# Performance work log

Hardware: AMD Instinct MI355X
Metric: run time of the kernel (lower is better)

## Reference

```python
import jax, jax.numpy as jnp
import numpy as np

N_V, N_R = 50000, 500
E_VV, E_VI, E_IV = 400000, 100000, 100000
D_V, D_R = 6, 1
HID, HEADS, OUT = 32, 2, 64
L2 = HID * HEADS  # input dim of layer 2 = hidden_dim * heads = 64


def _gatv2(x_src, x_dst, src, dst, Wl, bl, Wr, br, att, bias, heads, outc, add_self_loops):
    """PyG GATv2Conv: e_ij = att . leaky_relu(Wl x_j + Wr x_i), softmax over dst segments,
    out_i = sum_j alpha_ij * (Wl x_j). add_self_loops also removes pre-existing self loops
    (emulated with a validity mask to keep static shapes)."""
    n_src, n_dst = x_src.shape[0], x_dst.shape[0]
    hl = (x_src @ Wl + bl).reshape(n_src, heads, outc)  # source projection (messages)
    hr = (x_dst @ Wr + br).reshape(n_dst, heads, outc)  # target projection
    if add_self_loops:
        n_loop = min(n_src, n_dst)  # PyG uses min over bipartite sizes
        loop = jnp.arange(n_loop)
        valid = jnp.concatenate([src != dst, jnp.ones((n_loop,), bool)])
        src = jnp.concatenate([src, loop])
        dst = jnp.concatenate([dst, loop])
    else:
        valid = jnp.ones(src.shape, bool)
    m_src = hl[src]                                        # [E, H, C]
    m_dst = hr[dst]                                        # [E, H, C]
    e = (jax.nn.leaky_relu(m_src + m_dst, 0.2) * att).sum(-1)  # [E, H]
    e_masked = jnp.where(valid[:, None], e, -jnp.inf)
    emax = jax.ops.segment_max(e_masked, dst, num_segments=n_dst)
    emax = jnp.where(jnp.isfinite(emax), emax, 0.0)
    w = jnp.where(valid[:, None], jnp.exp(e - emax[dst]), 0.0)
    denom = jax.ops.segment_sum(w, dst, num_segments=n_dst)
    alpha = w / (denom[dst] + 1e-16)                       # [E, H]
    out = jax.ops.segment_sum(alpha[..., None] * m_src, dst, num_segments=n_dst)
    return out.reshape(n_dst, heads * outc) + bias         # concat (heads=1: identity)


def _ln(x, w, b):
    mu = jnp.mean(x, -1, keepdims=True)
    var = jnp.mean((x - mu) ** 2, -1, keepdims=True)
    return (x - mu) * jax.lax.rsqrt(var + 1e-5) * w + b


def setup_inputs() -> dict:
    key = jax.random.key(0)
    ks = jax.random.split(key, 50)
    rn = lambda i, shape, s=0.1: jax.random.normal(ks[i], shape, jnp.float32) * s
    inp = dict(
        x_veh=jax.random.normal(ks[0], (N_V, D_V), jnp.float32),
        x_rsu=jax.random.normal(ks[1], (N_R, D_R), jnp.float32),
        ei_v2v=jax.random.randint(ks[2], (2, E_VV), 0, N_V),
        ei_v2i=jnp.stack([jax.random.randint(ks[3], (E_VI,), 0, N_V),
                          jax.random.randint(ks[4], (E_VI,), 0, N_R)]),
        ei_i2v=jnp.stack([jax.random.randint(ks[5], (E_IV,), 0, N_R),
                          jax.random.randint(ks[6], (E_IV,), 0, N_V)]),
        # conv1 (heads=2, concat=True)
        p1v_Wl=rn(7, (D_V, L2)), p1v_bl=rn(8, (L2,)), p1v_Wr=rn(9, (D_V, L2)), p1v_br=rn(10, (L2,)), p1v_att=rn(11, (HEADS, HID)), p1v_b=rn(12, (L2,)),
        p1i_Wl=rn(13, (D_V, L2)), p1i_bl=rn(14, (L2,)), p1i_Wr=rn(15, (D_R, L2)), p1i_br=rn(16, (L2,)), p1i_att=rn(17, (HEADS, HID)), p1i_b=rn(18, (L2,)),
        p1r_Wl=rn(19, (D_R, L2)), p1r_bl=rn(20, (L2,)), p1r_Wr=rn(21, (D_V, L2)), p1r_br=rn(22, (L2,)), p1r_att=rn(23, (HEADS, HID)), p1r_b=rn(24, (L2,)),
        # conv2 (heads=1, concat=False)
        p2v_Wl=rn(25, (L2, OUT)), p2v_bl=rn(26, (OUT,)), p2v_Wr=rn(27, (L2, OUT)), p2v_br=rn(28, (OUT,)), p2v_att=rn(29, (1, OUT)), p2v_b=rn(30, (OUT,)),
        p2i_Wl=rn(31, (L2, OUT)), p2i_bl=rn(32, (OUT,)), p2i_Wr=rn(33, (L2, OUT)), p2i_br=rn(34, (OUT,)), p2i_att=rn(35, (1, OUT)), p2i_b=rn(36, (OUT,)),
        p2r_Wl=rn(37, (L2, OUT)), p2r_bl=rn(38, (OUT,)), p2r_Wr=rn(39, (L2, OUT)), p2r_br=rn(40, (OUT,)), p2r_att=rn(41, (1, OUT)), p2r_b=rn(42, (OUT,)),
        lnv_w=jnp.ones((OUT,), jnp.float32), lnv_b=jnp.zeros((OUT,), jnp.float32),
        lnr_w=jnp.ones((OUT,), jnp.float32), lnr_b=jnp.zeros((OUT,), jnp.float32),
    )
    return inp


def reference(x_veh, x_rsu, ei_v2v, ei_v2i, ei_i2v,
              p1v_Wl, p1v_bl, p1v_Wr, p1v_br, p1v_att, p1v_b,
              p1i_Wl, p1i_bl, p1i_Wr, p1i_br, p1i_att, p1i_b,
              p1r_Wl, p1r_bl, p1r_Wr, p1r_br, p1r_att, p1r_b,
              p2v_Wl, p2v_bl, p2v_Wr, p2v_br, p2v_att, p2v_b,
              p2i_Wl, p2i_bl, p2i_Wr, p2i_br, p2i_att, p2i_b,
              p2r_Wl, p2r_bl, p2r_Wr, p2r_br, p2r_att, p2r_b,
              lnv_w, lnv_b, lnr_w, lnr_b):
    # ---- HeteroConv layer 1 (aggr='sum') ----
    v_v2v = _gatv2(x_veh, x_veh, ei_v2v[0], ei_v2v[1], p1v_Wl, p1v_bl, p1v_Wr, p1v_br, p1v_att, p1v_b, HEADS, HID, True)
    r_v2i = _gatv2(x_veh, x_rsu, ei_v2i[0], ei_v2i[1], p1i_Wl, p1i_bl, p1i_Wr, p1i_br, p1i_att, p1i_b, HEADS, HID, False)
    v_i2v = _gatv2(x_rsu, x_veh, ei_i2v[0], ei_i2v[1], p1r_Wl, p1r_bl, p1r_Wr, p1r_br, p1r_att, p1r_b, HEADS, HID, False)
    h_veh = jax.nn.elu(v_v2v + v_i2v)
    h_rsu = jax.nn.elu(r_v2i)
    # dropout(p=0.2) is identity in eval mode
    # ---- HeteroConv layer 2 (heads=1, add_self_loops default True) ----
    v2 = (_gatv2(h_veh, h_veh, ei_v2v[0], ei_v2v[1], p2v_Wl, p2v_bl, p2v_Wr, p2v_br, p2v_att, p2v_b, 1, OUT, True)
          + _gatv2(h_rsu, h_veh, ei_i2v[0], ei_i2v[1], p2r_Wl, p2r_bl, p2r_Wr, p2r_br, p2r_att, p2r_b, 1, OUT, True))
    r2 = _gatv2(h_veh, h_rsu, ei_v2i[0], ei_v2i[1], p2i_Wl, p2i_bl, p2i_Wr, p2i_br, p2i_att, p2i_b, 1, OUT, True)
    return _ln(v2, lnv_w, lnv_b), _ln(r2, lnr_w, lnr_b)
```

## Files before the change

kernel.cpp:

```cpp
#include <hip/hip_runtime.h>
#include <hip/hip_fp16.h>
#include <math.h>
#include <float.h>

#define NV 50000
#define NR 500
#define EVV 400000
#define EVI 100000
#define EIV 100000

#define CB_VV 0
#define CB_VI 50000
#define CB_IV 50500
#define CNT_LEN 100500
#define RB_VV 0
#define RB_VI 50004
#define RB_IV 50508
#define RP_LEN 100512
#define TILE 1024
#define T_VV 49
#define T_IV 49
#define T_TOT 99
#define HB4 586
#define FB4 586
#define PB 12500
#define GBV 2048
#define NBQ 1563
#define RSB 16

__global__ void hist_all_kernel(const int* __restrict__ vv_s, const int* __restrict__ vv_d,
                                const int* __restrict__ vi_d, const int* __restrict__ iv_d,
                                unsigned* __restrict__ cnt_all, unsigned* __restrict__ rank_all) {
  int t0 = blockIdx.x * 1024 + threadIdx.x;
  #pragma unroll
  for (int j = 0; j < 4; ++j) {
    int e = t0 + j * 256;
    if (e < EVV) {
      int s = vv_s[e], d = vv_d[e];
      if (s != d) rank_all[e] = atomicAdd(&cnt_all[CB_VV + d], 1u);
    } else if (e < EVV + EVI) {
      rank_all[e] = atomicAdd(&cnt_all[CB_VI + vi_d[e - EVV]], 1u);
    } else if (e < EVV + EVI + EIV) {
      rank_all[e] = atomicAdd(&cnt_all[CB_IV + iv_d[e - EVV - EVI]], 1u);
    }
  }
}

__device__ __forceinline__ void tile_decode(int b, int& cb, int& rb, int& n, int& base,
                                            int& topo, int& lt) {
  topo = (b < T_VV) ? 0 : (b == T_VV) ? 1 : 2;
  lt   = (topo == 0) ? b : (topo == 1) ? 0 : b - T_VV - 1;
  cb   = (topo == 0) ? CB_VV : (topo == 1) ? CB_VI : CB_IV;
  rb   = (topo == 0) ? RB_VV : (topo == 1) ? RB_VI : RB_IV;
  n    = (topo == 1) ? NR : NV;
  base = lt * TILE;
}

__global__ void tilesum_kernel(const unsigned* __restrict__ cnt_all, unsigned* __restrict__ tsum) {
  int cb, rb, n, base, topo, lt;
  tile_decode(blockIdx.x, cb, rb, n, base, topo, lt);
  int t = threadIdx.x, lane = t & 63, wid = t >> 6;
  unsigned s = 0;
  #pragma unroll
  for (int j = 0; j < 4; ++j) {
    int i = base + t + j * 256;
    if (i < n) s += cnt_all[cb + i];
  }
  #pragma unroll
  for (int off = 32; off > 0; off >>= 1) s += (unsigned)__shfl_xor((int)s, off, 64);
  __shared__ unsigned wt[4];
  if (lane == 0) wt[wid] = s;
  __syncthreads();
  if (t == 0) tsum[blockIdx.x] = wt[0] + wt[1] + wt[2] + wt[3];
}

__global__ void scanwrite_kernel(const unsigned* __restrict__ cnt_all,
                                 const unsigned* __restrict__ tsum,
                                 unsigned* __restrict__ rp_all) {
  int cb, rb, n, base, topo, lt;
  tile_decode(blockIdx.x, cb, rb, n, base, topo, lt);
  int t = threadIdx.x, lane = t & 63, wid = t >> 6;
  __shared__ unsigned sprefix;
  __shared__ unsigned wt[4];
  if (wid == 0) {
    int first = (topo == 0) ? 0 : (topo == 1) ? T_VV : T_VV + 1;
    int cntT  = (topo == 1) ? 1 : T_VV;
    unsigned tv = (lane < cntT) ? tsum[first + lane] : 0u;
    unsigned vp = (lane < lt) ? tv : 0u;
    unsigned vt = tv;
    #pragma unroll
    for (int off = 32; off > 0; off >>= 1) {
      vp += (unsigned)__shfl_xor((int)vp, off, 64);
      vt += (unsigned)__shfl_xor((int)vt, off, 64);
    }
    if (lane == 0) {
      sprefix = vp;
      if (lt == 0) rp_all[rb + n] = vt;
    }
  }
  int i0 = base + t * 4;
  unsigned c0 = 0, c1 = 0, c2 = 0, c3 = 0;
  if (i0 + 3 < n) {
    uint4 v = *(const uint4*)&cnt_all[cb + i0];
    c0 = v.x; c1 = v.y; c2 = v.z; c3 = v.w;
  } else if (i0 < n) {
    c0 = cnt_all[cb + i0];
    if (i0 + 1 < n) c1 = cnt_all[cb + i0 + 1];
    if (i0 + 2 < n) c2 = cnt_all[cb + i0 + 2];
  }
  unsigned s4 = c0 + c1 + c2 + c3;
  unsigned inc = s4;
  #pragma unroll
  for (int off = 1; off < 64; off <<= 1) {
    unsigned v = (unsigned)__shfl_up((int)inc, off, 64);
    if (lane >= off) inc += v;
  }
  if (lane == 63) wt[wid] = inc;
  __syncthreads();
  unsigned wb = sprefix;
  #pragma unroll
  for (int w = 0; w < 4; ++w) if (w < wid) wb += wt[w];
  unsigned p0 = wb + inc - s4;
  unsigned p1 = p0 + c0, p2 = p1 + c1, p3 = p2 + c2;
  if (i0 + 3 < n) {
    *(uint4*)&rp_all[rb + i0] = make_uint4(p0, p1, p2, p3);
  } else if (i0 < n) {
    rp_all[rb + i0] = p0;
    if (i0 + 1 < n) rp_all[rb + i0 + 1] = p1;
    if (i0 + 2 < n) rp_all[rb + i0 + 2] = p2;
  }
}

__global__ void fill_proj_kernel(const int* __restrict__ vv_s, const int* __restrict__ vv_d,
                                 const int* __restrict__ vi_s, const int* __restrict__ vi_d,
                                 const int* __restrict__ iv_s, const int* __restrict__ iv_d,
                                 const unsigned* __restrict__ rp_all,
                                 const unsigned* __restrict__ rank_all,
                                 int* __restrict__ src_all,
                                 const float* __restrict__ x,
                                 const float* __restrict__ W0, const float* __restrict__ b0,
                                 const float* __restrict__ W1, const float* __restrict__ b1,
                                 const float* __restrict__ W2, const float* __restrict__ b2,
                                 const float* __restrict__ W3, const float* __restrict__ b3,
                                 __half* __restrict__ out0, __half* __restrict__ out1,
                                 float* __restrict__ out2, float* __restrict__ out3) {
  if (blockIdx.x < FB4) {
    int t0 = blockIdx.x * 1024 + threadIdx.x;
    #pragma unroll
    for (int j = 0; j < 4; ++j) {
      int e = t0 + j * 256;
      if (e < EVV) {
        int s = vv_s[e], d = vv_d[e];
        if (s != d) {
          unsigned pos = rp_all[RB_VV + d] + rank_all[e];
          __builtin_nontemporal_store(s, &src_all[pos]);
        }
      } else if (e < EVV + EVI) {
        int i = e - EVV;
        unsigned pos = rp_all[RB_VI + vi_d[i]] + rank_all[e];
        __builtin_nontemporal_store(vi_s[i], &src_all[EVV + pos]);
      } else if (e < EVV + EVI + EIV) {
        int i = e - EVV - EVI;
        unsigned pos = rp_all[RB_IV + iv_d[i]] + rank_all[e];
        __builtin_nontemporal_store(iv_s[i], &src_all[EVV + EVI + pos]);
      }
    }
  } else {
    int t = (blockIdx.x - FB4) * 256 + threadIdx.x;
    if (t >= NV * 64) return;
    int row = t >> 6, c = t & 63;
    const float* xr = x + (size_t)row * 6;
    float x0 = xr[0], x1 = xr[1], x2 = xr[2], x3 = xr[3], x4 = xr[4], x5 = xr[5];
    float a0 = b0[c], a1 = b1[c], a2 = b2[c], a3 = b3[c];
    a0 = fmaf(x0, W0[0 * 64 + c], a0); a1 = fmaf(x0, W1[0 * 64 + c], a1);
    a2 = fmaf(x0, W2[0 * 64 + c], a2); a3 = fmaf(x0, W3[0 * 64 + c], a3);
    a0 = fmaf(x1, W0[1 * 64 + c], a0); a1 = fmaf(x1, W1[1 * 64 + c], a1);
    a2 = fmaf(x1, W2[1 * 64 + c], a2); a3 = fmaf(x1, W3[1 * 64 + c], a3);
    a0 = fmaf(x2, W0[2 * 64 + c], a0); a1 = fmaf(x2, W1[2 * 64 + c], a1);
    a2 = fmaf(x2, W2[2 * 64 + c], a2); a3 = fmaf(x2, W3[2 * 64 + c], a3);
    a0 = fmaf(x3, W0[3 * 64 + c], a0); a1 = fmaf(x3, W1[3 * 64 + c], a1);
    a2 = fmaf(x3, W2[3 * 64 + c], a2); a3 = fmaf(x3, W3[3 * 64 + c], a3);
    a0 = fmaf(x4, W0[4 * 64 + c], a0); a1 = fmaf(x4, W1[4 * 64 + c], a1);
    a2 = fmaf(x4, W2[4 * 64 + c], a2); a3 = fmaf(x4, W3[4 * 64 + c], a3);
    a0 = fmaf(x5, W0[5 * 64 + c], a0); a1 = fmaf(x5, W1[5 * 64 + c], a1);
    a2 = fmaf(x5, W2[5 * 64 + c], a2); a3 = fmaf(x5, W3[5 * 64 + c], a3);
    out0[t] = __float2half(a0);
    out1[t] = __float2half(a1);
    out2[t] = a2;
    out3[t] = a3;
  }
}

template <int R0>
__device__ __forceinline__ float redsum(float ee) {
  #pragma unroll
  for (int off = R0; off > 0; off >>= 1) ee += __shfl_xor(ee, off, 64);
  return ee;
}

__device__ __forceinline__ float4 cvt_h(int2 r) {
  __half2 ab = *(__half2*)&r.x;
  __half2 cd = *(__half2*)&r.y;
  float2 f0 = __half22float2(ab);
  float2 f1 = __half22float2(cd);
  return make_float4(f0.x, f0.y, f1.x, f1.y);
}
__device__ __forceinline__ float4 ldrow_h(const __half* p) { return cvt_h(*(const int2*)p); }

__device__ __forceinline__ void merge_groups(float& s, float4& a) {
  s   += __shfl_xor(s, 16, 64);
  a.x += __shfl_xor(a.x, 16, 64);
  a.y += __shfl_xor(a.y, 16, 64);
  a.z += __shfl_xor(a.z, 16, 64);
  a.w += __shfl_xor(a.w, 16, 64);
  s   += __shfl_xor(s, 32, 64);
  a.x += __shfl_xor(a.x, 32, 64);
  a.y += __shfl_xor(a.y, 32, 64);
  a.z += __shfl_xor(a.z, 32, 64);
  a.w += __shfl_xor(a.w, 32, 64);
}

template <int R0>
__device__ __forceinline__ void edge_acc(float4 p4, bool ok, float4 h, float4 a,
                                         float& s, float4& acc) {
  float vx = p4.x + h.x; vx = fmaxf(vx, 0.2f * vx);
  float vy = p4.y + h.y; vy = fmaxf(vy, 0.2f * vy);
  float vz = p4.z + h.z; vz = fmaxf(vz, 0.2f * vz);
  float vw = p4.w + h.w; vw = fmaxf(vw, 0.2f * vw);
  float ee = redsum<R0>(fmaf(vx, a.x, fmaf(vy, a.y, fmaf(vz, a.z, vw * a.w))));
  float w = ok ? __expf(ee) : 0.f;
  s += w;
  acc.x = fmaf(w, p4.x, acc.x);
  acc.y = fmaf(w, p4.y, acc.y);
  acc.z = fmaf(w, p4.z, acc.z);
  acc.w = fmaf(w, p4.w, acc.w);
}

template <int CHUNK, int NSLOT, int R0, bool MASK>
__device__ __forceinline__ void gat4_table(unsigned beg, unsigned end, unsigned slot,
                                           const int* __restrict__ srcs,
                                           const __half* __restrict__ tab, int q, int d,
                                           float4 h, float4 a, float& s, float4& acc) {
  for (unsigned i = beg + slot; i < end; i += NSLOT * CHUNK) {
    float4 p[CHUNK]; bool ok[CHUNK];
    #pragma unroll
    for (int j = 0; j < CHUNK; ++j) {
      unsigned idx = i + (unsigned)(j * NSLOT);
      int sv = (idx < end) ? srcs[idx] : 0;
      ok[j] = (idx < end) && (!MASK || sv != d);
      p[j] = ldrow_h(tab + (size_t)sv * 64 + 4 * q);
    }
    #pragma unroll
    for (int j = 0; j < CHUNK; ++j) edge_acc<R0>(p[j], ok[j], h, a, s, acc);
  }
}

__global__ __launch_bounds__(256)
void l1_all_kernel(const unsigned* __restrict__ rp_all, const int* __restrict__ src_all,
                   const __half* __restrict__ TA, const __half* __restrict__ TB,
                   const float* __restrict__ HRVV, const float* __restrict__ HRIV,
                   const float* __restrict__ x_rsu,
                   const float* __restrict__ Wl_iv, const float* __restrict__ bl_iv,
                   const float* __restrict__ att_vv, const float* __restrict__ att_iv,
                   const float* __restrict__ Wr_vi, const float* __restrict__ br_vi,
                   const float* __restrict__ att_vi,
                   const float* __restrict__ b_vv, const float* __restrict__ b_iv,
                   const float* __restrict__ b_vi,
                   float* __restrict__ ACCV, float* __restrict__ ACCR) {
  __shared__ float sS[4][64];
  __shared__ float4 sA[4][64];
  int tid = threadIdx.x, lane = tid & 63, wid = tid >> 6;
  int q = lane & 15, g = lane >> 4;
  if (blockIdx.x < GBV) {
    float4 av = *(const float4*)&att_vv[4 * q];
    float4 ai = *(const float4*)&att_iv[4 * q];
    float4 wli = *(const float4*)&Wl_iv[4 * q];
    float4 bli = *(const float4*)&bl_iv[4 * q];
    float4 bvv = *(const float4*)&b_vv[4 * q];
    float4 biv = *(const float4*)&b_iv[4 * q];
    float4 bb = make_float4(bvv.x + biv.x, bvv.y + biv.y, bvv.z + biv.z, bvv.w + biv.w);
    const int* src_iv = src_all + EVV + EVI;
    int d = blockIdx.x * 4 + wid;
    unsigned vb = 0, ve = 0, ib = 0, ie = 0;
    int psv0 = 0, psv1 = 0, pisv = 0;
    if (d < NV) {
      vb = rp_all[RB_VV + d]; ve = rp_all[RB_VV + d + 1];
      ib = rp_all[RB_IV + d]; ie = rp_all[RB_IV + d + 1];
      unsigned i0 = vb + (unsigned)g, i1 = i0 + 4;
      psv0 = (i0 < ve) ? src_all[i0] : 0;
      psv1 = (i1 < ve) ? src_all[i1] : 0;
      unsigned ii0 = ib + (unsigned)g;
      pisv = (ii0 < ie) ? src_iv[ii0] : 0;
    }
    while (d < NV) {
      int dn = d + GBV * 4;
      unsigned cvb = vb, cve = ve, cib = ib, cie = ie;
      int2 r0raw = *(const int2*)(TA + (size_t)psv0 * 64 + 4 * q);
      int2 r1raw = *(const int2*)(TA + (size_t)psv1 * 64 + 4 * q);
      float ixv = x_rsu[pisv];
      bool iok0 = (cib + (unsigned)g) < cie;
      if (dn < NV) {
        vb = rp_all[RB_VV + dn]; ve = rp_all[RB_VV + dn + 1];
        ib = rp_all[RB_IV + dn]; ie = rp_all[RB_IV + dn + 1];
      }
      float4 hv = *(const float4*)&HRVV[(size_t)d * 64 + 4 * q];
      float4 hi = *(const float4*)&HRIV[(size_t)d * 64 + 4 * q];
      float sv_ = 0.f; float4 av_ = make_float4(0.f, 0.f, 0.f, 0.f);
      edge_acc<4>(cvt_h(r0raw), (cvb + (unsigned)g) < cve, hv, av, sv_, av_);
      edge_acc<4>(cvt_h(r1raw), (cvb + (unsigned)g + 4) < cve, hv, av, sv_, av_);
      gat4_table<2, 4, 4, false>(cvb + 8, cve, (unsigned)g, src_all, TA, q, d, hv, av, sv_, av_);
      if (g == 0) {
        float4 p4 = ldrow_h(TA + (size_t)d * 64 + 4 * q);
        edge_acc<4>(p4, true, hv, av, sv_, av_);
      }
      merge_groups(sv_, av_);
      float si_ = 0.f; float4 ai_ = make_float4(0.f, 0.f, 0.f, 0.f);
      {
        float4 p4;
        p4.x = fmaf(ixv, wli.x, bli.x);
        p4.y = fmaf(ixv, wli.y, bli.y);
        p4.z = fmaf(ixv, wli.z, bli.z);
        p4.w = fmaf(ixv, wli.w, bli.w);
        edge_acc<4>(p4, iok0, hi, ai, si_, ai_);
      }
      for (unsigned i = cib + 4 + (unsigned)g; i < cie; i += 4) {
        int sv2 = src_iv[i];
        float xv2 = x_rsu[sv2];
        float4 p4;
        p4.x = fmaf(xv2, wli.x, bli.x);
        p4.y = fmaf(xv2, wli.y, bli.y);
        p4.z = fmaf(xv2, wli.z, bli.z);
        p4.w = fmaf(xv2, wli.w, bli.w);
        edge_acc<4>(p4, true, hi, ai, si_, ai_);
      }
      merge_groups(si_, ai_);
      if (dn < NV) {
        unsigned i0 = vb + (unsigned)g, i1 = i0 + 4;
        psv0 = (i0 < ve) ? src_all[i0] : 0;
        psv1 = (i1 < ve) ? src_all[i1] : 0;
        unsigned ii0 = ib + (unsigned)g;
        pisv = (ii0 < ie) ? src_iv[ii0] : 0;
      }
      if (g == 0) {
        float rv = 1.f / (sv_ + 1e-16f), ri = 1.f / (si_ + 1e-16f);
        float v0 = av_.x * rv + ai_.x * ri + bb.x;
        float v1 = av_.y * rv + ai_.y * ri + bb.y;
        float v2 = av_.z * rv + ai_.z * ri + bb.z;
        float v3 = av_.w * rv + ai_.w * ri + bb.w;
        float4 o;
        o.x = (v0 > 0.f) ? v0 : expm1f(v0);
        o.y = (v1 > 0.f) ? v1 : expm1f(v1);
        o.z = (v2 > 0.f) ? v2 : expm1f(v2);
        o.w = (v3 > 0.f) ? v3 : expm1f(v3);
        *(float4*)&ACCV[(size_t)d * 64 + 4 * q] = o;
      }
      d = dn;
    }
  } else {
    int d = (int)blockIdx.x - GBV;
    float xv = x_rsu[d];
    float4 wrv = *(const float4*)&Wr_vi[4 * q];
    float4 brv = *(const float4*)&br_vi[4 * q];
    float4 h;
    h.x = fmaf(xv, wrv.x, brv.x);
    h.y = fmaf(xv, wrv.y, brv.y);
    h.z = fmaf(xv, wrv.z, brv.z);
    h.w = fmaf(xv, wrv.w, brv.w);
    float4 a = *(const float4*)&att_vi[4 * q];
    float s_ = 0.f; float4 a_ = make_float4(0.f, 0.f, 0.f, 0.f);
    gat4_table<4, 16, 4, false>(rp_all[RB_VI + d], rp_all[RB_VI + d + 1],
                                (unsigned)(wid * 4 + g), src_all + EVV, TB, q, d,
                                h, a, s_, a_);
    merge_groups(s_, a_);
    if (wid != 0) { sS[wid][lane] = s_; sA[wid][lane] = a_; }
    __syncthreads();
    if (wid == 0) {
      #pragma unroll
      for (int w2 = 1; w2 < 4; ++w2) {
        s_ += sS[w2][lane];
        float4 t = sA[w2][lane];
        a_.x += t.x; a_.y += t.y; a_.z += t.z; a_.w += t.w;
      }
      if (g == 0) {
        float4 bvi = *(const float4*)&b_vi[4 * q];
        float inv = 1.f / (s_ + 1e-16f);
        float v0 = a_.x * inv + bvi.x;
        float v1 = a_.y * inv + bvi.y;
        float v2 = a_.z * inv + bvi.z;
        float v3 = a_.w * inv + bvi.w;
        float4 o;
        o.x = (v0 > 0.f) ? v0 : expm1f(v0);
        o.y = (v1 > 0.f) ? v1 : expm1f(v1);
        o.z = (v2 > 0.f) ? v2 : expm1f(v2);
        o.w = (v3 > 0.f) ? v3 : expm1f(v3);
        *(float4*)&ACCR[(size_t)d * 64 + 4 * q] = o;
      }
    }
  }
}

__global__ __launch_bounds__(256, 2)
void quad_proj_kernel(const float* __restrict__ ACCVin, const float* __restrict__ ACCR,
                      const float* __restrict__ W0, const float* __restrict__ b0,
                      const float* __restrict__ W1, const float* __restrict__ b1,
                      const float* __restrict__ W2, const float* __restrict__ b2,
                      const float* __restrict__ W3, const float* __restrict__ b3,
                      const float* __restrict__ W4, const float* __restrict__ b4,
                      const float* __restrict__ W5, const float* __restrict__ b5,
                      __half* __restrict__ O0, float* __restrict__ O1,
                      float* __restrict__ O2, __half* __restrict__ O3,
                      __half* __restrict__ S0o, float* __restrict__ S1o) {
  __shared__ float w0s[4096], w1s[4096], w2s[4096], w3s[4096], xtile[2048];
  int t = threadIdx.x;
  bool vehb = blockIdx.x < NBQ;
  const float* X = vehb ? ACCVin : ACCR;
  int n = vehb ? NV : NR;
  int base = (vehb ? (int)blockIdx.x : (int)blockIdx.x - NBQ) * 32;
  if (vehb) {
    for (int i = t; i < 4096; i += 256) { w0s[i] = W0[i]; w1s[i] = W1[i]; w2s[i] = W2[i]; w3s[i] = W3[i]; }
  } else {
    for (int i = t; i < 4096; i += 256) { w0s[i] = W4[i]; w1s[i] = W5[i]; }
  }
  for (int i = t; i < 2048; i += 256) {
    int row = base + (i >> 6);
    int rc = (row < n) ? row : (n - 1);
    xtile[i] = X[(size_t)rc * 64 + (i & 63)];
  }
  __syncthreads();
  int lane = t & 63, wid = t >> 6;
  int wr = wid * 8;
  int p = 4 * (lane & 15) + (lane >> 4);
  if (vehb) {
    float a0[8], a1[8], a2[8], a3[8];
    #pragma unroll
    for (int r = 0; r < 8; ++r) { a0[r] = 0.f; a1[r] = 0.f; a2[r] = 0.f; a3[r] = 0.f; }
    for (int kq = 0; kq < 16; ++kq) {
      int k = kq * 4;
      float u00 = w0s[(k + 0) * 64 + lane], u01 = w0s[(k + 1) * 64 + lane];
      float u02 = w0s[(k + 2) * 64 + lane], u03 = w0s[(k + 3) * 64 + lane];
      float u10 = w1s[(k + 0) * 64 + lane], u11 = w1s[(k + 1) * 64 + lane];
      float u12 = w1s[(k + 2) * 64 + lane], u13 = w1s[(k + 3) * 64 + lane];
      float u20 = w2s[(k + 0) * 64 + lane], u21 = w2s[(k + 1) * 64 + lane];
      float u22 = w2s[(k + 2) * 64 + lane], u23 = w2s[(k + 3) * 64 + lane];
      float u30 = w3s[(k + 0) * 64 + lane], u31 = w3s[(k + 1) * 64 + lane];
      float u32 = w3s[(k + 2) * 64 + lane], u33 = w3s[(k + 3) * 64 + lane];
      #pragma unroll
      for (int r = 0; r < 8; ++r) {
        float4 xv = *(const float4*)&xtile[(wr + r) * 64 + k];
        a0[r] = fmaf(xv.x, u00, a0[r]); a0[r] = fmaf(xv.y, u01, a0[r]);
        a0[r] = fmaf(xv.z, u02, a0[r]); a0[r] = fmaf(xv.w, u03, a0[r]);
        a1[r] = fmaf(xv.x, u10, a1[r]); a1[r] = fmaf(xv.y, u11, a1[r]);
        a1[r] = fmaf(xv.z, u12, a1[r]); a1[r] = fmaf(xv.w, u13, a1[r]);
        a2[r] = fmaf(xv.x, u20, a2[r]); a2[r] = fmaf(xv.y, u21, a2[r]);
        a2[r] = fmaf(xv.z, u22, a2[r]); a2[r] = fmaf(xv.w, u23, a2[r]);
        a3[r] = fmaf(xv.x, u30, a3[r]); a3[r] = fmaf(xv.y, u31, a3[r]);
        a3[r] = fmaf(xv.z, u32, a3[r]); a3[r] = fmaf(xv.w, u33, a3[r]);
      }
    }
    float c0 = b0[lane], c1 = b1[lane], c2 = b2[lane], c3 = b3[lane];
    #pragma unroll
    for (int r = 0; r < 8; ++r) {
      int row = base + wr + r;
      if (row < n) {
        O0[(size_t)row * 64 + p] = __float2half(a0[r] + c0);
        O1[(size_t)row * 64 + p] = a1[r] + c1;
        O2[(size_t)row * 64 + p] = a2[r] + c2;
        O3[(size_t)row * 64 + p] = __float2half(a3[r] + c3);
      }
    }
  } else {
    float a0[8], a1[8];
    #pragma unroll
    for (int r = 0; r < 8; ++r) { a0[r] = 0.f; a1[r] = 0.f; }
    for (int kq = 0; kq < 16; ++kq) {
      int k = kq * 4;
      float u00 = w0s[(k + 0) * 64 + lane], u01 = w0s[(k + 1) * 64 + lane];
      float u02 = w0s[(k + 2) * 64 + lane], u03 = w0s[(k + 3) * 64 + lane];
      float u10 = w1s[(k + 0) * 64 + lane], u11 = w1s[(k + 1) * 64 + lane];
      float u12 = w1s[(k + 2) * 64 + lane], u13 = w1s[(k + 3) * 64 + lane];
      #pragma unroll
      for (int r = 0; r < 8; ++r) {
        float4 xv = *(const float4*)&xtile[(wr + r) * 64 + k];
        a0[r] = fmaf(xv.x, u00, a0[r]); a0[r] = fmaf(xv.y, u01, a0[r]);
        a0[r] = fmaf(xv.z, u02, a0[r]); a0[r] = fmaf(xv.w, u03, a0[r]);
        a1[r] = fmaf(xv.x, u10, a1[r]); a1[r] = fmaf(xv.y, u11, a1[r]);
        a1[r] = fmaf(xv.z, u12, a1[r]); a1[r] = fmaf(xv.w, u13, a1[r]);
      }
    }
    float c0 = b4[lane], c1 = b5[lane];
    #pragma unroll
    for (int r = 0; r < 8; ++r) {
      int row = base + wr + r;
      if (row < n) {
        S0o[(size_t)row * 64 + p] = __float2half(a0[r] + c0);
        S1o[(size_t)row * 64 + p] = a1[r] + c1;
      }
    }
  }
}

__global__ __launch_bounds__(256)
void l2_all_kernel(const unsigned* __restrict__ rp_all, const int* __restrict__ src_all,
                   const __half* __restrict__ Tvvl, const float* __restrict__ Tvvr,
                   const __half* __restrict__ Tivl, const float* __restrict__ Tivr,
                   const __half* __restrict__ Tvil, const float* __restrict__ Tvir,
                   const float* __restrict__ att_vv, const float* __restrict__ att_iv,
                   const float* __restrict__ att_vi,
                   const float* __restrict__ b_vv, const float* __restrict__ b_iv,
                   const float* __restrict__ b_vi,
                   const float* __restrict__ lnv_w, const float* __restrict__ lnv_b,
                   const float* __restrict__ lnr_w, const float* __restrict__ lnr_b,
                   float* __restrict__ outv, float* __restrict__ outr) {
  __shared__ float sS[4][64];
  __shared__ float4 sA[4][64];
  int tid = threadIdx.x, lane = tid & 63, wid = tid >> 6;
  int q = lane & 15, g = lane >> 4;
  if (blockIdx.x < GBV) {
    float4 av = make_float4(att_vv[q], att_vv[q + 16], att_vv[q + 32], att_vv[q + 48]);
    float4 ai = make_float4(att_iv[q], att_iv[q + 16], att_iv[q + 32], att_iv[q + 48]);
    float4 bb = make_float4(b_vv[q] + b_iv[q], b_vv[q + 16] + b_iv[q + 16],
                            b_vv[q + 32] + b_iv[q + 32], b_vv[q + 48] + b_iv[q + 48]);
    float4 lw = make_float4(lnv_w[q], lnv_w[q + 16], lnv_w[q + 32], lnv_w[q + 48]);
    float4 lb = make_float4(lnv_b[q], lnv_b[q + 16], lnv_b[q + 32], lnv_b[q + 48]);
    const int* src_iv = src_all + EVV + EVI;
    int d = blockIdx.x * 4 + wid;
    unsigned vb = 0, ve = 0, ib = 0, ie = 0;
    int psv0 = 0, psv1 = 0, pisv = 0;
    if (d < NV) {
      vb = rp_all[RB_VV + d]; ve = rp_all[RB_VV + d + 1];
      ib = rp_all[RB_IV + d]; ie = rp_all[RB_IV + d + 1];
      unsigned i0 = vb + (unsigned)g, i1 = i0 + 4;
      psv0 = (i0 < ve) ? src_all[i0] : 0;
      psv1 = (i1 < ve) ? src_all[i1] : 0;
      unsigned ii0 = ib + (unsigned)g;
      pisv = (ii0 < ie) ? src_iv[ii0] : 0;
    }
    while (d < NV) {
      int dn = d + GBV * 4;
      unsigned cvb = vb, cve = ve, cib = ib, cie = ie;
      int cisv = pisv;
      int2 r0raw = *(const int2*)(Tvvl + (size_t)psv0 * 64 + 4 * q);
      int2 r1raw = *(const int2*)(Tvvl + (size_t)psv1 * 64 + 4 * q);
      int2 ipraw = *(const int2*)(Tivl + (size_t)cisv * 64 + 4 * q);
      bool iok0 = (cib + (unsigned)g) < cie;
      if (dn < NV) {
        vb = rp_all[RB_VV + dn]; ve = rp_all[RB_VV + dn + 1];
        ib = rp_all[RB_IV + dn]; ie = rp_all[RB_IV + dn + 1];
      }
      float4 hv = *(const float4*)&Tvvr[(size_t)d * 64 + 4 * q];
      float4 hi = *(const float4*)&Tivr[(size_t)d * 64 + 4 * q];
      float sv_ = 0.f; float4 av_ = make_float4(0.f, 0.f, 0.f, 0.f);
      edge_acc<8>(cvt_h(r0raw), (cvb + (unsigned)g) < cve, hv, av, sv_, av_);
      edge_acc<8>(cvt_h(r1raw), (cvb + (unsigned)g + 4) < cve, hv, av, sv_, av_);
      gat4_table<2, 4, 8, false>(cvb + 8, cve, (unsigned)g, src_all, Tvvl, q, d, hv, av, sv_, av_);
      if (g == 0) {
        float4 p4 = ldrow_h(Tvvl + (size_t)d * 64 + 4 * q);
        edge_acc<8>(p4, true, hv, av, sv_, av_);
      }
      merge_groups(sv_, av_);
      float si_ = 0.f; float4 ai_ = make_float4(0.f, 0.f, 0.f, 0.f);
      edge_acc<8>(cvt_h(ipraw), iok0 && (cisv != d), hi, ai, si_, ai_);
      for (unsigned i = cib + 4 + (unsigned)g; i < cie; i += 4) {
        int sv2 = src_iv[i];
        float4 p4 = ldrow_h(Tivl + (size_t)sv2 * 64 + 4 * q);
        edge_acc<8>(p4, sv2 != d, hi, ai, si_, ai_);
      }
      if (g == 0 && d < NR) {
        float4 p4 = ldrow_h(Tivl + (size_t)d * 64 + 4 * q);
        edge_acc<8>(p4, true, hi, ai, si_, ai_);
      }
      merge_groups(si_, ai_);
      if (dn < NV) {
        unsigned i0 = vb + (unsigned)g, i1 = i0 + 4;
        psv0 = (i0 < ve) ? src_all[i0] : 0;
        psv1 = (i1 < ve) ? src_all[i1] : 0;
        unsigned ii0 = ib + (unsigned)g;
        pisv = (ii0 < ie) ? src_iv[ii0] : 0;
      }
      float rv = 1.f / (sv_ + 1e-16f), ri = 1.f / (si_ + 1e-16f);
      float v0 = av_.x * rv + ai_.x * ri + bb.x;
      float v1 = av_.y * rv + ai_.y * ri + bb.y;
      float v2 = av_.z * rv + ai_.z * ri + bb.z;
      float v3 = av_.w * rv + ai_.w * ri + bb.w;
      float sum = redsum<8>(v0 + v1 + v2 + v3);
      float mu = sum * (1.f / 64.f);
      float d0 = v0 - mu, d1 = v1 - mu, d2 = v2 - mu, d3 = v3 - mu;
      float qq = redsum<8>(d0 * d0 + d1 * d1 + d2 * d2 + d3 * d3);
      float is = rsqrtf(qq * (1.f / 64.f) + 1e-5f);
      if (g == 0) {
        outv[(size_t)d * 64 + q]      = d0 * is * lw.x + lb.x;
        outv[(size_t)d * 64 + q + 16] = d1 * is * lw.y + lb.y;
        outv[(size_t)d * 64 + q + 32] = d2 * is * lw.z + lb.z;
        outv[(size_t)d * 64 + q + 48] = d3 * is * lw.w + lb.w;
      }
      d = dn;
    }
  } else {
    int d = (int)blockIdx.x - GBV;
    float4 h = *(const float4*)&Tvir[(size_t)d * 64 + 4 * q];
    float4 a = make_float4(att_vi[q], att_vi[q + 16], att_vi[q + 32], att_vi[q + 48]);
    float s_ = 0.f; float4 a_ = make_float4(0.f, 0.f, 0.f, 0.f);
    gat4_table<4, 16, 8, true>(rp_all[RB_VI + d], rp_all[RB_VI + d + 1],
                               (unsigned)(wid * 4 + g), src_all + EVV, Tvil, q, d,
                               h, a, s_, a_);
    if (wid == 0 && g == 0) {
      float4 p4 = ldrow_h(Tvil + (size_t)d * 64 + 4 * q);
      edge_acc<8>(p4, true, h, a, s_, a_);
    }
    merge_groups(s_, a_);
    if (wid != 0) { sS[wid][lane] = s_; sA[wid][lane] = a_; }
    __syncthreads();
    if (wid == 0) {
      #pragma unroll
      for (int w2 = 1; w2 < 4; ++w2) {
        s_ += sS[w2][lane];
        float4 t = sA[w2][lane];
        a_.x += t.x; a_.y += t.y; a_.z += t.z; a_.w += t.w;
      }
      float inv = 1.f / (s_ + 1e-16f);
      float v0 = a_.x * inv + b_vi[q];
      float v1 = a_.y * inv + b_vi[q + 16];
      float v2 = a_.z * inv + b_vi[q + 32];
      float v3 = a_.w * inv + b_vi[q + 48];
      float sum = redsum<8>(v0 + v1 + v2 + v3);
      float mu = sum * (1.f / 64.f);
      float d0 = v0 - mu, d1 = v1 - mu, d2 = v2 - mu, d3 = v3 - mu;
      float qq = redsum<8>(d0 * d0 + d1 * d1 + d2 * d2 + d3 * d3);
      float is = rsqrtf(qq * (1.f / 64.f) + 1e-5f);
      if (g == 0) {
        outr[(size_t)d * 64 + q]      = d0 * is * lnr_w[q] + lnr_b[q];
        outr[(size_t)d * 64 + q + 16] = d1 * is * lnr_w[q + 16] + lnr_b[q + 16];
        outr[(size_t)d * 64 + q + 32] = d2 * is * lnr_w[q + 32] + lnr_b[q + 32];
        outr[(size_t)d * 64 + q + 48] = d3 * is * lnr_w[q + 48] + lnr_b[q + 48];
      }
    }
  }
}

extern "C" void kernel_launch(void* const* d_in, const int* in_sizes, int n_in,
                              void* d_out, int out_size, void* d_ws, size_t ws_size,
                              hipStream_t stream) {
  const float* x_veh = (const float*)d_in[0];
  const float* x_rsu = (const float*)d_in[1];
  const int* ei_v2v = (const int*)d_in[2];
  const int* ei_v2i = (const int*)d_in[3];
  const int* ei_i2v = (const int*)d_in[4];
  const float* P[36];
  for (int i = 0; i < 36; ++i) P[i] = (const float*)d_in[5 + i];
  const float* lnv_w = (const float*)d_in[41];
  const float* lnv_b = (const float*)d_in[42];
  const float* lnr_w = (const float*)d_in[43];
  const float* lnr_b = (const float*)d_in[44];

  float* ws = (float*)d_ws;
  float* P0    = ws;
  float* P1    = P0 + 3200000;
  float* ACCV  = P1 + 3200000;
  float* ACC2V = ACCV + 3200000;
  float* S0    = ACC2V + 3200000;
  float* S1    = S0 + 32000;
  float* ACCR  = S1 + 32000;
  unsigned* cnt_all    = (unsigned*)(ACCR + 32000);
  unsigned* rp_all     = cnt_all + CNT_LEN;
  unsigned* tsum       = rp_all + RP_LEN;
  unsigned* rank_all   = tsum + 128;
  int* src_all         = (int*)(rank_all + 600000);
  __half* TA_h   = (__half*)ACC2V;
  __half* TB_h   = (__half*)(ACC2V + 1600000);
  float*  HRVV   = P1;
  float*  HRIV   = P0;
  __half* Tvvl_h = (__half*)P0;
  __half* Tvil_h = (__half*)(P0 + 1600000);
  __half* Tivl_h = (__half*)S0;

  hipMemsetAsync(cnt_all, 0, (size_t)CNT_LEN * 4, stream);
  hist_all_kernel<<<HB4, 256, 0, stream>>>(
      ei_v2v, ei_v2v + EVV, ei_v2i + EVI, ei_i2v + EIV, cnt_all, rank_all);
  tilesum_kernel<<<T_TOT, 256, 0, stream>>>(cnt_all, tsum);
  scanwrite_kernel<<<T_TOT, 256, 0, stream>>>(cnt_all, tsum, rp_all);
  fill_proj_kernel<<<FB4 + PB, 256, 0, stream>>>(
      ei_v2v, ei_v2v + EVV, ei_v2i, ei_v2i + EVI, ei_i2v, ei_i2v + EIV,
      rp_all, rank_all, src_all,
      x_veh, P[0], P[1], P[6], P[7], P[2], P[3], P[14], P[15],
      TA_h, TB_h, HRVV, HRIV);

  l1_all_kernel<<<GBV + NR, 256, 0, stream>>>(
      rp_all, src_all, TA_h, TB_h, HRVV, HRIV, x_rsu,
      P[12], P[13],
      P[4], P[16],
      P[8], P[9], P[10],
      P[5], P[17], P[11],
      ACCV, ACCR);

  quad_proj_kernel<<<NBQ + RSB, 256, 0, stream>>>(
      ACCV, ACCR,
      P[18], P[19],
      P[20], P[21],
      P[32], P[33],
      P[24], P[25],
      P[30], P[31],
      P[26], P[27],
      Tvvl_h, P1, ACC2V, Tvil_h, Tivl_h, S1);

  l2_all_kernel<<<GBV + NR, 256, 0, stream>>>(
      rp_all, src_all,
      Tvvl_h, P1, Tivl_h, ACC2V, Tvil_h, S1,
      P[22], P[34], P[28],
      P[23], P[35], P[29],
      lnv_w, lnv_b, lnr_w, lnr_b,
      (float*)d_out, (float*)d_out + (size_t)NV * 64);
}
```

Before: 225.1 us.

## Replicate CSR degree histogram into eight copies to reduce atomic contention

The per-destination degree histogram is split into eight replicas, each chosen by block index, so atomics on hot destinations such as the 500 RSU nodes spread across more addresses. The scan sums the replicas and writes a per-replica exclusive offset array, which the fill kernel adds when placing each edge. This cuts atomic serialization at the cost of eight times the memset and extra reads in the scan and fill passes. It also reuses the ACCV workspace for the replicas.

```diff
diff --git a/kernel.cpp b/kernel.cpp
--- a/kernel.cpp
+++ b/kernel.cpp
@@ -13,6 +13,7 @@
 #define CB_VI 50000
 #define CB_IV 50500
 #define CNT_LEN 100500
+#define NREP 8
 #define RB_VV 0
 #define RB_VI 50004
 #define RB_IV 50508
@@ -21,7 +22,7 @@
 #define T_VV 49
 #define T_IV 49
 #define T_TOT 99
-#define HB4 586
+#define HB1 2344
 #define FB4 586
 #define PB 12500
 #define GBV 2048
@@ -30,19 +31,16 @@
 
 __global__ void hist_all_kernel(const int* __restrict__ vv_s, const int* __restrict__ vv_d,
                                 const int* __restrict__ vi_d, const int* __restrict__ iv_d,
-                                unsigned* __restrict__ cnt_all, unsigned* __restrict__ rank_all) {
-  int t0 = blockIdx.x * 1024 + threadIdx.x;
-  #pragma unroll
-  for (int j = 0; j < 4; ++j) {
-    int e = t0 + j * 256;
-    if (e < EVV) {
-      int s = vv_s[e], d = vv_d[e];
-      if (s != d) rank_all[e] = atomicAdd(&cnt_all[CB_VV + d], 1u);
-    } else if (e < EVV + EVI) {
-      rank_all[e] = atomicAdd(&cnt_all[CB_VI + vi_d[e - EVV]], 1u);
-    } else if (e < EVV + EVI + EIV) {
-      rank_all[e] = atomicAdd(&cnt_all[CB_IV + iv_d[e - EVV - EVI]], 1u);
-    }
+                                unsigned* __restrict__ cnt_rep, unsigned* __restrict__ rank_all) {
+  int e = blockIdx.x * 256 + threadIdx.x;
+  unsigned rbase = (unsigned)(blockIdx.x & (NREP - 1)) * CNT_LEN;
+  if (e < EVV) {
+    int s = vv_s[e], d = vv_d[e];
+    if (s != d) rank_all[e] = atomicAdd(&cnt_rep[rbase + CB_VV + d], 1u);
+  } else if (e < EVV + EVI) {
+    rank_all[e] = atomicAdd(&cnt_rep[rbase + CB_VI + vi_d[e - EVV]], 1u);
+  } else if (e < EVV + EVI + EIV) {
+    rank_all[e] = atomicAdd(&cnt_rep[rbase + CB_IV + iv_d[e - EVV - EVI]], 1u);
   }
 }
 
@@ -56,7 +54,7 @@
   base = lt * TILE;
 }
 
-__global__ void tilesum_kernel(const unsigned* __restrict__ cnt_all, unsigned* __restrict__ tsum) {
+__global__ void tilesum_kernel(const unsigned* __restrict__ cnt_rep, unsigned* __restrict__ tsum) {
   int cb, rb, n, base, topo, lt;
   tile_decode(blockIdx.x, cb, rb, n, base, topo, lt);
   int t = threadIdx.x, lane = t & 63, wid = t >> 6;
@@ -64,7 +62,10 @@
   #pragma unroll
   for (int j = 0; j < 4; ++j) {
     int i = base + t + j * 256;
-    if (i < n) s += cnt_all[cb + i];
+    if (i < n) {
+      #pragma unroll
+      for (int r = 0; r < NREP; ++r) s += cnt_rep[r * CNT_LEN + cb + i];
+    }
   }
   #pragma unroll
   for (int off = 32; off > 0; off >>= 1) s += (unsigned)__shfl_xor((int)s, off, 64);
@@ -74,9 +75,10 @@
   if (t == 0) tsum[blockIdx.x] = wt[0] + wt[1] + wt[2] + wt[3];
 }
 
-__global__ void scanwrite_kernel(const unsigned* __restrict__ cnt_all,
+__global__ void scanwrite_kernel(const unsigned* __restrict__ cnt_rep,
                                  const unsigned* __restrict__ tsum,
-                                 unsigned* __restrict__ rp_all) {
+                                 unsigned* __restrict__ rp_all,
+                                 unsigned* __restrict__ roff) {
   int cb, rb, n, base, topo, lt;
   tile_decode(blockIdx.x, cb, rb, n, base, topo, lt);
   int t = threadIdx.x, lane = t & 63, wid = t >> 6;
@@ -99,16 +101,21 @@
     }
   }
   int i0 = base + t * 4;
-  unsigned c0 = 0, c1 = 0, c2 = 0, c3 = 0;
-  if (i0 + 3 < n) {
-    uint4 v = *(const uint4*)&cnt_all[cb + i0];
-    c0 = v.x; c1 = v.y; c2 = v.z; c3 = v.w;
-  } else if (i0 < n) {
-    c0 = cnt_all[cb + i0];
-    if (i0 + 1 < n) c1 = cnt_all[cb + i0 + 1];
-    if (i0 + 2 < n) c2 = cnt_all[cb + i0 + 2];
-  }
-  unsigned s4 = c0 + c1 + c2 + c3;
+  unsigned c[4] = {0u, 0u, 0u, 0u};
+  #pragma unroll
+  for (int j = 0; j < 4; ++j) {
+    int i = i0 + j;
+    if (i < n) {
+      unsigned acc = 0;
+      #pragma unroll
+      for (int r = 0; r < NREP; ++r) {
+        roff[r * CNT_LEN + cb + i] = acc;
+        acc += cnt_rep[r * CNT_LEN + cb + i];
+      }
+      c[j] = acc;
+    }
+  }
+  unsigned s4 = c[0] + c[1] + c[2] + c[3];
   unsigned inc = s4;
   #pragma unroll
   for (int off = 1; off < 64; off <<= 1) {
@@ -121,7 +128,7 @@
   #pragma unroll
   for (int w = 0; w < 4; ++w) if (w < wid) wb += wt[w];
   unsigned p0 = wb + inc - s4;
-  unsigned p1 = p0 + c0, p2 = p1 + c1, p3 = p2 + c2;
+  unsigned p1 = p0 + c[0], p2 = p1 + c[1], p3 = p2 + c[2];
   if (i0 + 3 < n) {
     *(uint4*)&rp_all[rb + i0] = make_uint4(p0, p1, p2, p3);
   } else if (i0 < n) {
@@ -135,6 +142,7 @@
                                  const int* __restrict__ vi_s, const int* __restrict__ vi_d,
                                  const int* __restrict__ iv_s, const int* __restrict__ iv_d,
                                  const unsigned* __restrict__ rp_all,
+                                 const unsigned* __restrict__ roff,
                                  const unsigned* __restrict__ rank_all,
                                  int* __restrict__ src_all,
                                  const float* __restrict__ x,
@@ -149,19 +157,22 @@
     #pragma unroll
     for (int j = 0; j < 4; ++j) {
       int e = t0 + j * 256;
+      unsigned rb2 = (unsigned)((e >> 8) & (NREP - 1)) * CNT_LEN;
       if (e < EVV) {
         int s = vv_s[e], d = vv_d[e];
         if (s != d) {
-          unsigned pos = rp_all[RB_VV + d] + rank_all[e];
+          unsigned pos = rp_all[RB_VV + d] + roff[rb2 + CB_VV + d] + rank_all[e];
           __builtin_nontemporal_store(s, &src_all[pos]);
         }
       } else if (e < EVV + EVI) {
         int i = e - EVV;
-        unsigned pos = rp_all[RB_VI + vi_d[i]] + rank_all[e];
+        int d = vi_d[i];
+        unsigned pos = rp_all[RB_VI + d] + roff[rb2 + CB_VI + d] + rank_all[e];
         __builtin_nontemporal_store(vi_s[i], &src_all[EVV + pos]);
       } else if (e < EVV + EVI + EIV) {
         int i = e - EVV - EVI;
-        unsigned pos = rp_all[RB_IV + iv_d[i]] + rank_all[e];
+        int d = iv_d[i];
+        unsigned pos = rp_all[RB_IV + d] + roff[rb2 + CB_IV + d] + rank_all[e];
         __builtin_nontemporal_store(iv_s[i], &src_all[EVV + EVI + pos]);
       }
     }
@@ -660,11 +671,12 @@
   float* S0    = ACC2V + 3200000;
   float* S1    = S0 + 32000;
   float* ACCR  = S1 + 32000;
-  unsigned* cnt_all    = (unsigned*)(ACCR + 32000);
-  unsigned* rp_all     = cnt_all + CNT_LEN;
+  unsigned* rp_all     = (unsigned*)(ACCR + 32000);
   unsigned* tsum       = rp_all + RP_LEN;
   unsigned* rank_all   = tsum + 128;
   int* src_all         = (int*)(rank_all + 600000);
+  unsigned* cnt_rep    = (unsigned*)ACCV;
+  unsigned* roff       = cnt_rep + NREP * CNT_LEN;
   __half* TA_h   = (__half*)ACC2V;
   __half* TB_h   = (__half*)(ACC2V + 1600000);
   float*  HRVV   = P1;
@@ -673,14 +685,14 @@
   __half* Tvil_h = (__half*)(P0 + 1600000);
   __half* Tivl_h = (__half*)S0;
 
-  hipMemsetAsync(cnt_all, 0, (size_t)CNT_LEN * 4, stream);
-  hist_all_kernel<<<HB4, 256, 0, stream>>>(
-      ei_v2v, ei_v2v + EVV, ei_v2i + EVI, ei_i2v + EIV, cnt_all, rank_all);
-  tilesum_kernel<<<T_TOT, 256, 0, stream>>>(cnt_all, tsum);
-  scanwrite_kernel<<<T_TOT, 256, 0, stream>>>(cnt_all, tsum, rp_all);
+  hipMemsetAsync(cnt_rep, 0, (size_t)NREP * CNT_LEN * 4, stream);
+  hist_all_kernel<<<HB1, 256, 0, stream>>>(
+      ei_v2v, ei_v2v + EVV, ei_v2i + EVI, ei_i2v + EIV, cnt_rep, rank_all);
+  tilesum_kernel<<<T_TOT, 256, 0, stream>>>(cnt_rep, tsum);
+  scanwrite_kernel<<<T_TOT, 256, 0, stream>>>(cnt_rep, tsum, rp_all, roff);
   fill_proj_kernel<<<FB4 + PB, 256, 0, stream>>>(
       ei_v2v, ei_v2v + EVV, ei_v2i, ei_v2i + EVI, ei_i2v, ei_i2v + EIV,
-      rp_all, rank_all, src_all,
+      rp_all, roff, rank_all, src_all,
       x_veh, P[0], P[1], P[6], P[7], P[2], P[3], P[14], P[15],
       TA_h, TB_h, HRVV, HRIV);
 
```

Result: faster. 210.2 us (-6.6%).
